# Kernel optimization log

Measured on AMD Instinct MI355X. Metric: run time of the kernel, lower is better.

The kernel has to match this reference:

```python
import jax, jax.numpy as jnp
import numpy as np
from jax import lax

B, CIN, N = 4, 3, 2048
H, COUT, LEVELS = 128, 3, 3
HEADS = 8

# jnp.convolve(x, f, 'same') with len(f)=8 == correlation with f[::-1], x zero-padded (4,3).
# DWT then takes [::2], which is conv stride 2. IDWT zero-upsamples (lhs_dilation=2) then
# convolves 'same' with f[::-1], i.e. correlation with f, padding (4,4).

def _dwt(x, wlow, whigh):
    # x: (M, L) -> approx, detail each (M, L//2)
    rhs = jnp.stack([wlow[::-1], whigh[::-1]])[:, None, :]  # (2,1,8)
    out = lax.conv_general_dilated(x[:, None, :], rhs, window_strides=(2,),
                                   padding=[(4, 3)],
                                   dimension_numbers=('NCH', 'OIH', 'NCH'))
    return out[:, 0, :], out[:, 1, :]

def _idwt(a, d, wlow, whigh):
    # a, d: (M, L) -> (M, 2L); recon_low + recon_high fused as a 2-in-channel conv
    lhs = jnp.stack([a, d], axis=1)               # (M,2,L)
    rhs = jnp.stack([wlow, whigh])[None, :, :]    # (1,2,8)
    out = lax.conv_general_dilated(lhs, rhs, window_strides=(1,),
                                   padding=[(4, 4)], lhs_dilation=(2,),
                                   dimension_numbers=('NCH', 'OIH', 'NCH'))
    return out[:, 0, :]


def setup_inputs() -> dict:
    key = jax.random.key(0)
    ks = jax.random.split(key, 12)
    db4_low = jnp.array([0.23037781, 0.71484657, 0.63088076, -0.02798376,
                         -0.18703481, 0.03084138, 0.03288301, -0.0105974], jnp.float32)
    db4_high = jnp.array([-0.0105974, -0.03288301, 0.03084138, 0.18703481,
                          -0.02798376, -0.63088076, 0.71484657, -0.23037781], jnp.float32)
    def s(k, shape, fan_in):
        return jax.random.normal(k, shape, jnp.float32) * (1.0 / fan_in) ** 0.5
    return {
        'x': jax.random.normal(ks[0], (B, CIN, N), jnp.float32),
        'wlow': db4_low, 'whigh': db4_high,
        'Win': s(ks[1], (CIN, H), CIN), 'b_in': jnp.zeros((H,), jnp.float32),
        'W1': s(ks[2], (LEVELS, 2, 2 * H), 2), 'b1': jnp.zeros((LEVELS, 2 * H), jnp.float32),
        'W2': s(ks[3], (LEVELS, 2 * H, H), 2 * H), 'b2': jnp.zeros((LEVELS, H), jnp.float32),
        'Wq': s(ks[4], (H, H), H), 'bq': jnp.zeros((H,), jnp.float32),
        'Wk': s(ks[5], (H, H), H), 'bk': jnp.zeros((H,), jnp.float32),
        'Wv': s(ks[6], (H, H), H), 'bv': jnp.zeros((H,), jnp.float32),
        'Wo': s(ks[7], (H, H), H), 'bo': jnp.zeros((H,), jnp.float32),
        'Wout': s(ks[8], (H, COUT), H), 'bout': jnp.zeros((COUT,), jnp.float32),
    }


def reference(x, wlow, whigh, Win, b_in, W1, b1, W2, b2,
              Wq, bq, Wk, bk, Wv, bv, Wo, bo, Wout, bout):
    Bx = x.shape[0]
    # input projection: (B,CIN,N) -> (B,H,N)
    xp = jnp.einsum('bcn,ch->bhn', x, Win) + b_in[None, :, None]
    cur = xp.reshape(Bx * H, N)  # per-(batch,channel) 1D signals, fully batched
    proc = []  # processed coeffs per level; note approx == detail after the shared mean
    for lvl in range(LEVELS):
        a, d = _dwt(cur, wlow, whigh)                 # (M, L)
        c = jnp.stack([a, d], axis=-1)                # (M, L, 2)
        h = jax.nn.gelu(c @ W1[lvl] + b1[lvl])        # (M, L, 2H)
        p = (h @ W2[lvl] + b2[lvl]).mean(axis=-1)     # (M, L): mean over hidden dim
        proc.append(p)
        cur = a
    rec = proc[-1]  # start from deepest processed approx
    for lvl in range(LEVELS - 1, -1, -1):
        rec = _idwt(rec, proc[lvl], wlow, whigh)
    y = rec.reshape(Bx, H, N)
    # cross-level attention: standard MHA with embed_dim=H, 8 heads, no dropout
    seq = y.transpose(0, 2, 1)  # (B,N,H)
    dh = H // HEADS
    q = (seq @ Wq + bq).reshape(Bx, N, HEADS, dh)
    k = (seq @ Wk + bk).reshape(Bx, N, HEADS, dh)
    v = (seq @ Wv + bv).reshape(Bx, N, HEADS, dh)
    att = jnp.einsum('bqhd,bkhd->bhqk', q, k) * (dh ** -0.5)
    att = jax.nn.softmax(att, axis=-1)
    o = jnp.einsum('bhqk,bkhd->bqhd', att, v).reshape(Bx, N, H)
    o = o @ Wo + bo
    out = o @ Wout + bout  # (B,N,COUT)
    return out.transpose(0, 2, 1)  # (B,COUT,N)
```

## Files before the change

kernel.cpp:

```cpp
#include <hip/hip_runtime.h>

#define N_    2048
#define H_    128
#define B_    4
#define CIN_  3
#define COUT_ 3
#define LOG2E 1.44269504089f

__device__ __forceinline__ float gelu_tanh(float x) {
    float x2 = x * x;
    float e = __builtin_amdgcn_exp2f(x * fmaf(-0.10294340397f, x2, -2.30220899f));
    return x * __builtin_amdgcn_rcpf(1.0f + e);
}

__global__ void prep_kernel(const float* __restrict__ W1, const float* __restrict__ b1,
                            const float* __restrict__ W2, const float* __restrict__ b2,
                            const float* __restrict__ Wo, const float* __restrict__ bo,
                            const float* __restrict__ Wout, const float* __restrict__ bout,
                            float4* __restrict__ wpack, float* __restrict__ b2m,
                            float* __restrict__ wf, float* __restrict__ bf) {
    int gid = blockIdx.x * 256 + threadIdx.x;
    if (gid < 768) {
        const float* r = W2 + (size_t)gid * 128;
        float s = 0.f;
        for (int h = 0; h < 128; ++h) s += r[h];
        int lvl = gid >> 8, k = gid & 255;
        wpack[gid] = make_float4(W1[lvl * 512 + k], W1[lvl * 512 + 256 + k],
                                 b1[gid], s * (1.0f / 128.0f));
    } else if (gid < 771) {
        int lvl = gid - 768;
        const float* r = b2 + lvl * 128;
        float s = 0.f;
        for (int h = 0; h < 128; ++h) s += r[h];
        b2m[lvl] = s * (1.0f / 128.0f);
    } else if (gid >= 1024 && gid < 1408) {
        int e = gid - 1024;
        int h = e / 3, c = e - 3 * h;
        float s = 0.f;
        for (int j = 0; j < 128; ++j) s = fmaf(Wo[h * 128 + j], Wout[j * 3 + c], s);
        wf[e] = s;
    } else if (gid >= 1408 && gid < 1411) {
        int c = gid - 1408;
        float s = bout[c];
        for (int j = 0; j < 128; ++j) s = fmaf(bo[j], Wout[j * 3 + c], s);
        bf[c] = s;
    }
}

template<bool FUSEX>
__global__ __launch_bounds__(256) void dwt_mlp_kernel(
        const float* __restrict__ src, int loSh,
        const float* __restrict__ x, const float* __restrict__ Win,
        const float* __restrict__ b_in,
        const float* __restrict__ wlow, const float* __restrict__ whigh,
        const float4* __restrict__ wpack, const float* __restrict__ b2ml,
        float* __restrict__ a_out, float* __restrict__ p_out) {
    int tid = threadIdx.x;
    int gid = blockIdx.x * 256 + tid;
    int Lo  = 1 << loSh;
    int m   = gid >> loSh;
    int i   = gid & (Lo - 1);
    int L   = Lo << 1;
    int j0  = 2 * i - 4;
    float xw[8];
    if (FUSEX) {
        int b = m >> 7, h = m & 127;
        float w0 = Win[h], w1 = Win[128 + h], w2 = Win[256 + h];
        float bi = b_in[h];
        const float* xr = x + (size_t)b * (CIN_ * N_);
#pragma unroll
        for (int t = 0; t < 8; ++t) {
            int j = j0 + t;
            bool ok = (unsigned)j < (unsigned)L;
            int jc = ok ? j : 0;
            float v = bi;
            v = fmaf(xr[jc], w0, v);
            v = fmaf(xr[N_ + jc], w1, v);
            v = fmaf(xr[2 * N_ + jc], w2, v);
            xw[t] = ok ? v : 0.f;
        }
    } else {
        const float* row = src + (size_t)m * L;
#pragma unroll
        for (int t = 0; t < 8; ++t) {
            int j = j0 + t;
            xw[t] = ((unsigned)j < (unsigned)L) ? row[j] : 0.f;
        }
    }
    float a = 0.f, d = 0.f;
#pragma unroll
    for (int t = 0; t < 8; ++t) {
        a = fmaf(xw[t], wlow[7 - t], a);
        d = fmaf(xw[t], whigh[7 - t], d);
    }
    float acc = 0.f;
#pragma unroll 8
    for (int kk = 0; kk < 256; ++kk) {
        float4 w = wpack[kk];
        float t = fmaf(a, w.x, fmaf(d, w.y, w.z));
        acc = fmaf(gelu_tanh(t), w.w, acc);
    }
    a_out[gid] = a;
    p_out[gid] = acc + b2ml[0];
}

__global__ __launch_bounds__(256) void idwt_kernel(
        const float* __restrict__ aSrc, const float* __restrict__ dSrc,
        int loutSh, const float* __restrict__ wlow, const float* __restrict__ whigh,
        float* __restrict__ out) {
    int tid  = threadIdx.x;
    int gid  = blockIdx.x * 256 + tid;
    int Lout = 1 << loutSh;
    int L    = Lout >> 1;
    int m    = gid >> loutSh;
    int ii   = gid & (Lout - 1);
    const float* ar = aSrc + (size_t)m * L;
    const float* dr = dSrc + (size_t)m * L;
    int podd = ii & 1;
    int off0 = (ii >> 1) - 2 + podd;
    float wlp[4], whp[4];
#pragma unroll
    for (int s = 0; s < 4; ++s) {
        wlp[s] = podd ? wlow[2 * s + 1] : wlow[2 * s];
        whp[s] = podd ? whigh[2 * s + 1] : whigh[2 * s];
    }
    float r = 0.f;
#pragma unroll
    for (int s = 0; s < 4; ++s) {
        int idx = off0 + s;
        bool ok = (unsigned)idx < (unsigned)L;
        float av = ok ? ar[idx] : 0.f;
        float dv = ok ? dr[idx] : 0.f;
        r = fmaf(av, wlp[s], r);
        r = fmaf(dv, whp[s], r);
    }
    out[gid] = r;
}

__global__ __launch_bounds__(384) void qkv_kernel(
        const float* __restrict__ r0,
        const float* __restrict__ Wq, const float* __restrict__ bq,
        const float* __restrict__ Wk, const float* __restrict__ bk,
        const float* __restrict__ Wv, const float* __restrict__ bv,
        float* __restrict__ qB, float* __restrict__ kB, float* __restrict__ vB) {
    int tid = threadIdx.x;
    int rowbase = blockIdx.x * 16;
    int b  = rowbase >> 11;
    int n0 = rowbase & 2047;

    const float* W; const float* bias; float* dst; int jj;
    if (tid < 128)      { W = Wq; bias = bq; dst = qB; jj = tid; }
    else if (tid < 256) { W = Wk; bias = bk; dst = kB; jj = tid - 128; }
    else                { W = Wv; bias = bv; dst = vB; jj = tid - 256; }

    const float* abase = r0 + (size_t)b * (H_ * N_) + n0;
    float acc[16];
#pragma unroll
    for (int r = 0; r < 16; ++r) acc[r] = 0.f;
    for (int h = 0; h < 128; ++h) {
        float w = W[h * 128 + jj];
        const float* ar = abase + (size_t)h * N_;
#pragma unroll
        for (int r = 0; r < 16; ++r) acc[r] = fmaf(ar[r], w, acc[r]);
    }
    float bb = bias[jj];
    int head = jj >> 4, t = jj & 15;
    size_t obase = ((size_t)(b * 8 + head) * N_) * 16 + t;
#pragma unroll
    for (int r = 0; r < 16; ++r)
        dst[obase + (size_t)(n0 + r) * 16] = acc[r] + bb;
}

#define DOT4(acc, qq, aa) do { acc = fmaf(qq.x, aa.x, acc); acc = fmaf(qq.y, aa.y, acc); \
                               acc = fmaf(qq.z, aa.z, acc); acc = fmaf(qq.w, aa.w, acc); } while (0)
#define SCALE4(oo, c)     do { oo.x *= c; oo.y *= c; oo.z *= c; oo.w *= c; } while (0)
#define AXPY4(oo, p, aa)  do { oo.x = fmaf(p, aa.x, oo.x); oo.y = fmaf(p, aa.y, oo.y); \
                               oo.z = fmaf(p, aa.z, oo.z); oo.w = fmaf(p, aa.w, oo.w); } while (0)

template<int KS>
__global__ __launch_bounds__(128, 2) void attn_kernel(
        const float* __restrict__ qb, const float* __restrict__ kb,
        const float* __restrict__ vb,
        float* __restrict__ part_o, float* __restrict__ part_ml) {
    __shared__ float4 kt4[512];
    __shared__ float4 vt4[512];
    int tid   = threadIdx.x;
    int blk   = blockIdx.x;
    int split = blk % KS;
    int qblk  = (blk / KS) & 3;
    int bh    = blk / (4 * KS);

    const float4* ksrc = (const float4*)(kb + (size_t)bh * (N_ * 16));
    const float4* vsrc = (const float4*)(vb + (size_t)bh * (N_ * 16));
    const float sc = 0.25f * LOG2E;

    float4 q[4][4];
    float  m[4], l[4];
    float4 o[4][4];
#pragma unroll
    for (int qi = 0; qi < 4; ++qi) {
        const float4* qr = (const float4*)(qb + ((size_t)bh * N_ + qblk * 512 + qi * 128 + tid) * 16);
#pragma unroll
        for (int j = 0; j < 4; ++j) { q[qi][j] = qr[j]; SCALE4(q[qi][j], sc); }
        m[qi] = -3.0e38f; l[qi] = 0.f;
#pragma unroll
        for (int j = 0; j < 4; ++j) o[qi][j] = make_float4(0.f, 0.f, 0.f, 0.f);
    }

    int k0 = split * (N_ / KS);
    for (int t0 = k0; t0 < k0 + N_ / KS; t0 += 128) {
        __syncthreads();
        const float4* ks = ksrc + t0 * 4;
        const float4* vs = vsrc + t0 * 4;
#pragma unroll
        for (int u = 0; u < 4; ++u) {
            kt4[tid + u * 128] = ks[tid + u * 128];
            vt4[tid + u * 128] = vs[tid + u * 128];
        }
        __syncthreads();

        for (int c0 = 0; c0 < 128; c0 += 4) {
            float sv[4][4];
            float cm[4] = {-3.0e38f, -3.0e38f, -3.0e38f, -3.0e38f};
#pragma unroll
            for (int c = 0; c < 4; ++c) {
                int kr = (c0 + c) * 4;
                float4 k0v = kt4[kr], k1v = kt4[kr+1], k2v = kt4[kr+2], k3v = kt4[kr+3];
#pragma unroll
                for (int qi = 0; qi < 4; ++qi) {
                    float s0 = 0.f, s1 = 0.f;
                    DOT4(s0, q[qi][0], k0v); DOT4(s1, q[qi][1], k1v);
                    DOT4(s0, q[qi][2], k2v); DOT4(s1, q[qi][3], k3v);
                    sv[qi][c] = s0 + s1;
                    cm[qi] = fmaxf(cm[qi], sv[qi][c]);
                }
            }
            bool need = (cm[0] > m[0] + 8.f) || (cm[1] > m[1] + 8.f) ||
                        (cm[2] > m[2] + 8.f) || (cm[3] > m[3] + 8.f);
            if (__any(need)) {
#pragma unroll
                for (int qi = 0; qi < 4; ++qi) {
                    float mn = fmaxf(m[qi], cm[qi]);
                    float cr = __builtin_amdgcn_exp2f(m[qi] - mn);
                    l[qi] *= cr;
#pragma unroll
                    for (int j = 0; j < 4; ++j) SCALE4(o[qi][j], cr);
                    m[qi] = mn;
                }
            }
#pragma unroll
            for (int c = 0; c < 4; ++c) {
                int vr = (c0 + c) * 4;
                float4 v0 = vt4[vr], v1 = vt4[vr+1], v2 = vt4[vr+2], v3 = vt4[vr+3];
#pragma unroll
                for (int qi = 0; qi < 4; ++qi) {
                    float p = __builtin_amdgcn_exp2f(sv[qi][c] - m[qi]);
                    l[qi] += p;
                    AXPY4(o[qi][0], p, v0); AXPY4(o[qi][1], p, v1);
                    AXPY4(o[qi][2], p, v2); AXPY4(o[qi][3], p, v3);
                }
            }
        }
    }
#pragma unroll
    for (int qi = 0; qi < 4; ++qi) {
        int qg = bh * N_ + qblk * 512 + qi * 128 + tid;
        float4* po = (float4*)part_o + ((size_t)split * 65536 + qg) * 4;
        po[0] = o[qi][0]; po[1] = o[qi][1]; po[2] = o[qi][2]; po[3] = o[qi][3];
        ((float2*)part_ml)[(size_t)split * 65536 + qg] = make_float2(m[qi], l[qi]);
    }
}

template<int KS>
__global__ __launch_bounds__(512) void combine_final_kernel(
        const float* __restrict__ part_o, const float* __restrict__ part_ml,
        const float* __restrict__ wf, const float* __restrict__ bf,
        float* __restrict__ out) {
    __shared__ float ysh[64 * 129];
    int tid = threadIdx.x;
    int b = blockIdx.x >> 5, nb = blockIdx.x & 31;
    int head = tid >> 6, nl = tid & 63;
    int n = nb * 64 + nl;
    int qg = (b * 8 + head) * N_ + n;

    float m[KS], l[KS];
    float M = -3.0e38f;
#pragma unroll
    for (int s = 0; s < KS; ++s) {
        float2 ml = ((const float2*)part_ml)[(size_t)s * 65536 + qg];
        m[s] = ml.x; l[s] = ml.y;
        M = fmaxf(M, m[s]);
    }
    float w[KS], lt = 0.f;
#pragma unroll
    for (int s = 0; s < KS; ++s) {
        w[s] = __builtin_amdgcn_exp2f(m[s] - M);
        lt = fmaf(l[s], w[s], lt);
    }
    float inv = __builtin_amdgcn_rcpf(lt);
    float o[16];
#pragma unroll
    for (int j = 0; j < 16; ++j) o[j] = 0.f;
#pragma unroll
    for (int s = 0; s < KS; ++s) {
        const float4* po = (const float4*)part_o + ((size_t)s * 65536 + qg) * 4;
#pragma unroll
        for (int r = 0; r < 4; ++r) {
            float4 v = po[r];
            o[4*r+0] = fmaf(v.x, w[s], o[4*r+0]);
            o[4*r+1] = fmaf(v.y, w[s], o[4*r+1]);
            o[4*r+2] = fmaf(v.z, w[s], o[4*r+2]);
            o[4*r+3] = fmaf(v.w, w[s], o[4*r+3]);
        }
    }
    int col = head * 16;
#pragma unroll
    for (int j = 0; j < 16; ++j) ysh[nl * 129 + col + j] = o[j] * inv;
    __syncthreads();
    if (tid < 192) {
        int c = tid >> 6, nl2 = tid & 63;
        float acc = bf[c];
        const float* yr = ysh + nl2 * 129;
#pragma unroll 4
        for (int h = 0; h < 128; ++h) acc = fmaf(yr[h], wf[h * 3 + c], acc);
        out[((size_t)b * 3 + c) * N_ + nb * 64 + nl2] = acc;
    }
}

extern "C" void kernel_launch(void* const* d_in, const int* in_sizes, int n_in,
                              void* d_out, int out_size, void* d_ws, size_t ws_size,
                              hipStream_t stream) {
    const float* x    = (const float*)d_in[0];
    const float* wlow = (const float*)d_in[1];
    const float* whigh= (const float*)d_in[2];
    const float* Win  = (const float*)d_in[3];
    const float* b_in = (const float*)d_in[4];
    const float* W1   = (const float*)d_in[5];
    const float* b1   = (const float*)d_in[6];
    const float* W2   = (const float*)d_in[7];
    const float* b2   = (const float*)d_in[8];
    const float* Wq   = (const float*)d_in[9];
    const float* bq   = (const float*)d_in[10];
    const float* Wk   = (const float*)d_in[11];
    const float* bk   = (const float*)d_in[12];
    const float* Wv   = (const float*)d_in[13];
    const float* bv   = (const float*)d_in[14];
    const float* Wo   = (const float*)d_in[15];
    const float* bo   = (const float*)d_in[16];
    const float* Wout = (const float*)d_in[17];
    const float* bout = (const float*)d_in[18];
    float* out = (float*)d_out;
    (void)in_sizes; (void)n_in; (void)out_size;

    float* ws = (float*)d_ws;
    float* qBuf  = ws;
    float* kBuf  = ws + 1048576;
    float* vBuf  = ws + 2097152;
    float* base2 = ws + 3145728;
    float* a1 = base2;
    float* p0 = base2 + 524288;
    float* a2 = base2 + 1048576;
    float* p1 = base2 + 1310720;
    float* a3 = base2 + 1572864;
    float* p2 = base2 + 1703936;
    float* r2 = base2 + 1835008;
    float* r1 = base2 + 2097152;
    float* r0 = base2 + 2621440;

    const size_t need8 = (3145728ull + 8ull * 1048576 + 8ull * 131072 + 8192ull) * 4;
    int KS = (ws_size >= need8) ? 8 : 4;

    float* part_o  = base2;
    float* part_ml = base2 + (size_t)KS * 1048576;
    float* smalls  = part_ml + (size_t)KS * 131072;
    float4* wpack = (float4*)smalls;
    float* b2m = smalls + 3072;
    float* wf  = smalls + 3088;
    float* bf  = smalls + 3472;

    prep_kernel<<<8, 256, 0, stream>>>(W1, b1, W2, b2, Wo, bo, Wout, bout, wpack, b2m, wf, bf);

    dwt_mlp_kernel<true><<<2048, 256, 0, stream>>>(nullptr, 10, x, Win, b_in, wlow, whigh,
                                                   wpack + 0,   b2m + 0, a1, p0);
    dwt_mlp_kernel<false><<<1024, 256, 0, stream>>>(a1, 9, nullptr, nullptr, nullptr, wlow, whigh,
                                                    wpack + 256, b2m + 1, a2, p1);
    dwt_mlp_kernel<false><<<512, 256, 0, stream>>>(a2, 8, nullptr, nullptr, nullptr, wlow, whigh,
                                                   wpack + 512, b2m + 2, a3, p2);

    idwt_kernel<<<1024, 256, 0, stream>>>(p2, p2, 9,  wlow, whigh, r2);
    idwt_kernel<<<2048, 256, 0, stream>>>(r2, p1, 10, wlow, whigh, r1);
    idwt_kernel<<<4096, 256, 0, stream>>>(r1, p0, 11, wlow, whigh, r0);

    qkv_kernel<<<512, 384, 0, stream>>>(r0, Wq, bq, Wk, bk, Wv, bv, qBuf, kBuf, vBuf);

    if (KS == 8) {
        attn_kernel<8><<<32 * 4 * 8, 128, 0, stream>>>(qBuf, kBuf, vBuf, part_o, part_ml);
        combine_final_kernel<8><<<128, 512, 0, stream>>>(part_o, part_ml, wf, bf, out);
    } else {
        attn_kernel<4><<<32 * 4 * 4, 128, 0, stream>>>(qBuf, kBuf, vBuf, part_o, part_ml);
        combine_final_kernel<4><<<128, 512, 0, stream>>>(part_o, part_ml, wf, bf, out);
    }
}
```

Before: 358.4 us.

## Fuse wavelet DWT/MLP/IDWT levels into one kernel and restructure attention

Replaces the three DWT+MLP launches and three IDWT launches with a single kernel per (batch,channel) row that keeps all intermediate levels in shared memory and only writes the reconstructed row. Separately rewrites attention to use 64-thread blocks with two queries per thread, reading K/V rows directly from global memory instead of staging tiles in LDS. The fusion removes launch overhead and global round trips. The attention change trades LDS reuse and per-thread query reuse for more blocks and no barriers, which risks higher load traffic per key.

```diff
diff --git a/kernel.cpp b/kernel.cpp
--- a/kernel.cpp
+++ b/kernel.cpp
@@ -47,94 +47,175 @@
     }
 }
 
-template<bool FUSEX>
-__global__ __launch_bounds__(256) void dwt_mlp_kernel(
-        const float* __restrict__ src, int loSh,
+__global__ __launch_bounds__(256) void wavelet_fused_kernel(
         const float* __restrict__ x, const float* __restrict__ Win,
         const float* __restrict__ b_in,
         const float* __restrict__ wlow, const float* __restrict__ whigh,
-        const float4* __restrict__ wpack, const float* __restrict__ b2ml,
-        float* __restrict__ a_out, float* __restrict__ p_out) {
+        const float4* __restrict__ wpack, const float* __restrict__ b2m,
+        float* __restrict__ r0g) {
+    __shared__ float cur[2048];
+    __shared__ float aA[1024];
+    __shared__ float pp0[1024];
+    __shared__ float aB[512];
+    __shared__ float pp1[512];
+    __shared__ float pp2[256];
+    __shared__ float r2s[512];
+    __shared__ float r1s[1024];
     int tid = threadIdx.x;
-    int gid = blockIdx.x * 256 + tid;
-    int Lo  = 1 << loSh;
-    int m   = gid >> loSh;
-    int i   = gid & (Lo - 1);
-    int L   = Lo << 1;
-    int j0  = 2 * i - 4;
-    float xw[8];
-    if (FUSEX) {
-        int b = m >> 7, h = m & 127;
-        float w0 = Win[h], w1 = Win[128 + h], w2 = Win[256 + h];
-        float bi = b_in[h];
-        const float* xr = x + (size_t)b * (CIN_ * N_);
+    int m = blockIdx.x;
+    int b = m >> 7, h = m & 127;
+    float w0 = Win[h], w1 = Win[128 + h], w2 = Win[256 + h];
+    float bi = b_in[h];
+    float wl[8], wh[8];
+#pragma unroll
+    for (int t = 0; t < 8; ++t) { wl[t] = wlow[t]; wh[t] = whigh[t]; }
+
+    const float* xr = x + (size_t)b * (CIN_ * N_);
+    for (int idx = tid; idx < 2048; idx += 256) {
+        float v = bi;
+        v = fmaf(xr[idx], w0, v);
+        v = fmaf(xr[N_ + idx], w1, v);
+        v = fmaf(xr[2 * N_ + idx], w2, v);
+        cur[idx] = v;
+    }
+    __syncthreads();
+
+    {
+        float a4[4], d4[4], acc4[4];
+#pragma unroll
+        for (int u = 0; u < 4; ++u) {
+            int i = tid + u * 256;
+            int j0 = 2 * i - 4;
+            float a = 0.f, d = 0.f;
+#pragma unroll
+            for (int t = 0; t < 8; ++t) {
+                int j = j0 + t;
+                float xv = ((unsigned)j < 2048u) ? cur[j] : 0.f;
+                a = fmaf(xv, wl[7 - t], a);
+                d = fmaf(xv, wh[7 - t], d);
+            }
+            a4[u] = a; d4[u] = d; aA[i] = a; acc4[u] = 0.f;
+        }
+#pragma unroll 4
+        for (int kk = 0; kk < 256; ++kk) {
+            float4 w = wpack[kk];
+#pragma unroll
+            for (int u = 0; u < 4; ++u) {
+                float t = fmaf(a4[u], w.x, fmaf(d4[u], w.y, w.z));
+                acc4[u] = fmaf(gelu_tanh(t), w.w, acc4[u]);
+            }
+        }
+        float bb = b2m[0];
+#pragma unroll
+        for (int u = 0; u < 4; ++u) pp0[tid + u * 256] = acc4[u] + bb;
+    }
+    __syncthreads();
+
+    {
+        float a2v[2], d2v[2], acc2[2];
+#pragma unroll
+        for (int u = 0; u < 2; ++u) {
+            int i = tid + u * 256;
+            int j0 = 2 * i - 4;
+            float a = 0.f, d = 0.f;
+#pragma unroll
+            for (int t = 0; t < 8; ++t) {
+                int j = j0 + t;
+                float xv = ((unsigned)j < 1024u) ? aA[j] : 0.f;
+                a = fmaf(xv, wl[7 - t], a);
+                d = fmaf(xv, wh[7 - t], d);
+            }
+            a2v[u] = a; d2v[u] = d; aB[i] = a; acc2[u] = 0.f;
+        }
+#pragma unroll 4
+        for (int kk = 0; kk < 256; ++kk) {
+            float4 w = wpack[256 + kk];
+#pragma unroll
+            for (int u = 0; u < 2; ++u) {
+                float t = fmaf(a2v[u], w.x, fmaf(d2v[u], w.y, w.z));
+                acc2[u] = fmaf(gelu_tanh(t), w.w, acc2[u]);
+            }
+        }
+        float bb = b2m[1];
+#pragma unroll
+        for (int u = 0; u < 2; ++u) pp1[tid + u * 256] = acc2[u] + bb;
+    }
+    __syncthreads();
+
+    {
+        int j0 = 2 * tid - 4;
+        float a = 0.f, d = 0.f;
 #pragma unroll
         for (int t = 0; t < 8; ++t) {
             int j = j0 + t;
-            bool ok = (unsigned)j < (unsigned)L;
-            int jc = ok ? j : 0;
-            float v = bi;
-            v = fmaf(xr[jc], w0, v);
-            v = fmaf(xr[N_ + jc], w1, v);
-            v = fmaf(xr[2 * N_ + jc], w2, v);
-            xw[t] = ok ? v : 0.f;
-        }
-    } else {
-        const float* row = src + (size_t)m * L;
-#pragma unroll
-        for (int t = 0; t < 8; ++t) {
-            int j = j0 + t;
-            xw[t] = ((unsigned)j < (unsigned)L) ? row[j] : 0.f;
-        }
-    }
-    float a = 0.f, d = 0.f;
-#pragma unroll
-    for (int t = 0; t < 8; ++t) {
-        a = fmaf(xw[t], wlow[7 - t], a);
-        d = fmaf(xw[t], whigh[7 - t], d);
-    }
-    float acc = 0.f;
-#pragma unroll 8
-    for (int kk = 0; kk < 256; ++kk) {
-        float4 w = wpack[kk];
-        float t = fmaf(a, w.x, fmaf(d, w.y, w.z));
-        acc = fmaf(gelu_tanh(t), w.w, acc);
-    }
-    a_out[gid] = a;
-    p_out[gid] = acc + b2ml[0];
-}
-
-__global__ __launch_bounds__(256) void idwt_kernel(
-        const float* __restrict__ aSrc, const float* __restrict__ dSrc,
-        int loutSh, const float* __restrict__ wlow, const float* __restrict__ whigh,
-        float* __restrict__ out) {
-    int tid  = threadIdx.x;
-    int gid  = blockIdx.x * 256 + tid;
-    int Lout = 1 << loutSh;
-    int L    = Lout >> 1;
-    int m    = gid >> loutSh;
-    int ii   = gid & (Lout - 1);
-    const float* ar = aSrc + (size_t)m * L;
-    const float* dr = dSrc + (size_t)m * L;
-    int podd = ii & 1;
-    int off0 = (ii >> 1) - 2 + podd;
-    float wlp[4], whp[4];
-#pragma unroll
-    for (int s = 0; s < 4; ++s) {
-        wlp[s] = podd ? wlow[2 * s + 1] : wlow[2 * s];
-        whp[s] = podd ? whigh[2 * s + 1] : whigh[2 * s];
-    }
-    float r = 0.f;
-#pragma unroll
-    for (int s = 0; s < 4; ++s) {
-        int idx = off0 + s;
-        bool ok = (unsigned)idx < (unsigned)L;
-        float av = ok ? ar[idx] : 0.f;
-        float dv = ok ? dr[idx] : 0.f;
-        r = fmaf(av, wlp[s], r);
-        r = fmaf(dv, whp[s], r);
-    }
-    out[gid] = r;
+            float xv = ((unsigned)j < 512u) ? aB[j] : 0.f;
+            a = fmaf(xv, wl[7 - t], a);
+            d = fmaf(xv, wh[7 - t], d);
+        }
+        float acc = 0.f;
+#pragma unroll 4
+        for (int kk = 0; kk < 256; ++kk) {
+            float4 w = wpack[512 + kk];
+            float t = fmaf(a, w.x, fmaf(d, w.y, w.z));
+            acc = fmaf(gelu_tanh(t), w.w, acc);
+        }
+        pp2[tid] = acc + b2m[2];
+    }
+    __syncthreads();
+
+#pragma unroll
+    for (int u = 0; u < 2; ++u) {
+        int ii = tid + u * 256;
+        int podd = ii & 1;
+        int off0 = (ii >> 1) - 2 + podd;
+        float r = 0.f;
+#pragma unroll
+        for (int s = 0; s < 4; ++s) {
+            int idx = off0 + s;
+            float av = ((unsigned)idx < 256u) ? pp2[idx] : 0.f;
+            r = fmaf(av, wl[2 * s + podd] + wh[2 * s + podd], r);
+        }
+        r2s[ii] = r;
+    }
+    __syncthreads();
+
+#pragma unroll
+    for (int u = 0; u < 4; ++u) {
+        int ii = tid + u * 256;
+        int podd = ii & 1;
+        int off0 = (ii >> 1) - 2 + podd;
+        float r = 0.f;
+#pragma unroll
+        for (int s = 0; s < 4; ++s) {
+            int idx = off0 + s;
+            bool ok = (unsigned)idx < 512u;
+            float av = ok ? r2s[idx] : 0.f;
+            float dv = ok ? pp1[idx] : 0.f;
+            r = fmaf(av, wl[2 * s + podd], r);
+            r = fmaf(dv, wh[2 * s + podd], r);
+        }
+        r1s[ii] = r;
+    }
+    __syncthreads();
+
+    float* orow = r0g + (size_t)m * 2048;
+#pragma unroll
+    for (int u = 0; u < 8; ++u) {
+        int ii = tid + u * 256;
+        int podd = ii & 1;
+        int off0 = (ii >> 1) - 2 + podd;
+        float r = 0.f;
+#pragma unroll
+        for (int s = 0; s < 4; ++s) {
+            int idx = off0 + s;
+            bool ok = (unsigned)idx < 1024u;
+            float av = ok ? r1s[idx] : 0.f;
+            float dv = ok ? pp0[idx] : 0.f;
+            r = fmaf(av, wl[2 * s + podd], r);
+            r = fmaf(dv, wh[2 * s + podd], r);
+        }
+        orow[ii] = r;
+    }
 }
 
 __global__ __launch_bounds__(384) void qkv_kernel(
@@ -178,97 +259,66 @@
                                oo.z = fmaf(p, aa.z, oo.z); oo.w = fmaf(p, aa.w, oo.w); } while (0)
 
 template<int KS>
-__global__ __launch_bounds__(128, 2) void attn_kernel(
+__global__ __launch_bounds__(64, 3) void attn_kernel(
         const float* __restrict__ qb, const float* __restrict__ kb,
         const float* __restrict__ vb,
         float* __restrict__ part_o, float* __restrict__ part_ml) {
-    __shared__ float4 kt4[512];
-    __shared__ float4 vt4[512];
-    int tid   = threadIdx.x;
+    int lane  = threadIdx.x;
     int blk   = blockIdx.x;
     int split = blk % KS;
-    int qblk  = (blk / KS) & 3;
-    int bh    = blk / (4 * KS);
-
-    const float4* ksrc = (const float4*)(kb + (size_t)bh * (N_ * 16));
-    const float4* vsrc = (const float4*)(vb + (size_t)bh * (N_ * 16));
+    int qblk  = (blk / KS) & 15;
+    int bh    = blk / (16 * KS);
+    int nA    = qblk * 128 + lane;
+    int nB    = nA + 64;
+
     const float sc = 0.25f * LOG2E;
-
-    float4 q[4][4];
-    float  m[4], l[4];
-    float4 o[4][4];
-#pragma unroll
-    for (int qi = 0; qi < 4; ++qi) {
-        const float4* qr = (const float4*)(qb + ((size_t)bh * N_ + qblk * 512 + qi * 128 + tid) * 16);
-#pragma unroll
-        for (int j = 0; j < 4; ++j) { q[qi][j] = qr[j]; SCALE4(q[qi][j], sc); }
-        m[qi] = -3.0e38f; l[qi] = 0.f;
-#pragma unroll
-        for (int j = 0; j < 4; ++j) o[qi][j] = make_float4(0.f, 0.f, 0.f, 0.f);
-    }
-
+    const float4* qra = (const float4*)(qb + ((size_t)bh * N_ + nA) * 16);
+    const float4* qrb = (const float4*)(qb + ((size_t)bh * N_ + nB) * 16);
+    float4 qa0 = qra[0], qa1 = qra[1], qa2 = qra[2], qa3 = qra[3];
+    float4 qb0 = qrb[0], qb1 = qrb[1], qb2 = qrb[2], qb3 = qrb[3];
+    SCALE4(qa0, sc); SCALE4(qa1, sc); SCALE4(qa2, sc); SCALE4(qa3, sc);
+    SCALE4(qb0, sc); SCALE4(qb1, sc); SCALE4(qb2, sc); SCALE4(qb3, sc);
+
+    float mA = -3.0e38f, lA = 0.f, mB = -3.0e38f, lB = 0.f;
+    float4 oA0 = {0,0,0,0}, oA1 = oA0, oA2 = oA0, oA3 = oA0;
+    float4 oB0 = oA0, oB1 = oA0, oB2 = oA0, oB3 = oA0;
+
+    const float* kbase = kb + (size_t)bh * (N_ * 16);
+    const float* vbase = vb + (size_t)bh * (N_ * 16);
     int k0 = split * (N_ / KS);
-    for (int t0 = k0; t0 < k0 + N_ / KS; t0 += 128) {
-        __syncthreads();
-        const float4* ks = ksrc + t0 * 4;
-        const float4* vs = vsrc + t0 * 4;
-#pragma unroll
-        for (int u = 0; u < 4; ++u) {
-            kt4[tid + u * 128] = ks[tid + u * 128];
-            vt4[tid + u * 128] = vs[tid + u * 128];
-        }
-        __syncthreads();
-
-        for (int c0 = 0; c0 < 128; c0 += 4) {
-            float sv[4][4];
-            float cm[4] = {-3.0e38f, -3.0e38f, -3.0e38f, -3.0e38f};
-#pragma unroll
-            for (int c = 0; c < 4; ++c) {
-                int kr = (c0 + c) * 4;
-                float4 k0v = kt4[kr], k1v = kt4[kr+1], k2v = kt4[kr+2], k3v = kt4[kr+3];
-#pragma unroll
-                for (int qi = 0; qi < 4; ++qi) {
-                    float s0 = 0.f, s1 = 0.f;
-                    DOT4(s0, q[qi][0], k0v); DOT4(s1, q[qi][1], k1v);
-                    DOT4(s0, q[qi][2], k2v); DOT4(s1, q[qi][3], k3v);
-                    sv[qi][c] = s0 + s1;
-                    cm[qi] = fmaxf(cm[qi], sv[qi][c]);
-                }
-            }
-            bool need = (cm[0] > m[0] + 8.f) || (cm[1] > m[1] + 8.f) ||
-                        (cm[2] > m[2] + 8.f) || (cm[3] > m[3] + 8.f);
-            if (__any(need)) {
-#pragma unroll
-                for (int qi = 0; qi < 4; ++qi) {
-                    float mn = fmaxf(m[qi], cm[qi]);
-                    float cr = __builtin_amdgcn_exp2f(m[qi] - mn);
-                    l[qi] *= cr;
-#pragma unroll
-                    for (int j = 0; j < 4; ++j) SCALE4(o[qi][j], cr);
-                    m[qi] = mn;
-                }
-            }
-#pragma unroll
-            for (int c = 0; c < 4; ++c) {
-                int vr = (c0 + c) * 4;
-                float4 v0 = vt4[vr], v1 = vt4[vr+1], v2 = vt4[vr+2], v3 = vt4[vr+3];
-#pragma unroll
-                for (int qi = 0; qi < 4; ++qi) {
-                    float p = __builtin_amdgcn_exp2f(sv[qi][c] - m[qi]);
-                    l[qi] += p;
-                    AXPY4(o[qi][0], p, v0); AXPY4(o[qi][1], p, v1);
-                    AXPY4(o[qi][2], p, v2); AXPY4(o[qi][3], p, v3);
-                }
-            }
-        }
-    }
-#pragma unroll
-    for (int qi = 0; qi < 4; ++qi) {
-        int qg = bh * N_ + qblk * 512 + qi * 128 + tid;
-        float4* po = (float4*)part_o + ((size_t)split * 65536 + qg) * 4;
-        po[0] = o[qi][0]; po[1] = o[qi][1]; po[2] = o[qi][2]; po[3] = o[qi][3];
-        ((float2*)part_ml)[(size_t)split * 65536 + qg] = make_float2(m[qi], l[qi]);
-    }
+#pragma unroll 2
+    for (int t = k0; t < k0 + N_ / KS; ++t) {
+        const float4* kr = (const float4*)(kbase + (size_t)t * 16);
+        float4 k0v = kr[0], k1v = kr[1], k2v = kr[2], k3v = kr[3];
+        float sA0 = 0.f, sA1 = 0.f, sB0 = 0.f, sB1 = 0.f;
+        DOT4(sA0, qa0, k0v); DOT4(sA1, qa1, k1v); DOT4(sA0, qa2, k2v); DOT4(sA1, qa3, k3v);
+        DOT4(sB0, qb0, k0v); DOT4(sB1, qb1, k1v); DOT4(sB0, qb2, k2v); DOT4(sB1, qb3, k3v);
+        float sA = sA0 + sA1, sB = sB0 + sB1;
+        if (__any((sA > mA + 8.f) || (sB > mB + 8.f))) {
+            float mnA = fmaxf(mA, sA), mnB = fmaxf(mB, sB);
+            float cA = __builtin_amdgcn_exp2f(mA - mnA);
+            float cB = __builtin_amdgcn_exp2f(mB - mnB);
+            lA *= cA; lB *= cB;
+            SCALE4(oA0, cA); SCALE4(oA1, cA); SCALE4(oA2, cA); SCALE4(oA3, cA);
+            SCALE4(oB0, cB); SCALE4(oB1, cB); SCALE4(oB2, cB); SCALE4(oB3, cB);
+            mA = mnA; mB = mnB;
+        }
+        float pA = __builtin_amdgcn_exp2f(sA - mA);
+        float pB = __builtin_amdgcn_exp2f(sB - mB);
+        lA += pA; lB += pB;
+        const float4* vr = (const float4*)(vbase + (size_t)t * 16);
+        float4 v0 = vr[0], v1 = vr[1], v2 = vr[2], v3 = vr[3];
+        AXPY4(oA0, pA, v0); AXPY4(oA1, pA, v1); AXPY4(oA2, pA, v2); AXPY4(oA3, pA, v3);
+        AXPY4(oB0, pB, v0); AXPY4(oB1, pB, v1); AXPY4(oB2, pB, v2); AXPY4(oB3, pB, v3);
+    }
+
+    int qgA = bh * N_ + nA, qgB = bh * N_ + nB;
+    float4* poA = (float4*)part_o + ((size_t)split * 65536 + qgA) * 4;
+    poA[0] = oA0; poA[1] = oA1; poA[2] = oA2; poA[3] = oA3;
+    float4* poB = (float4*)part_o + ((size_t)split * 65536 + qgB) * 4;
+    poB[0] = oB0; poB[1] = oB1; poB[2] = oB2; poB[3] = oB3;
+    ((float2*)part_ml)[(size_t)split * 65536 + qgA] = make_float2(mA, lA);
+    ((float2*)part_ml)[(size_t)split * 65536 + qgB] = make_float2(mB, lB);
 }
 
 template<int KS>
@@ -357,17 +407,9 @@
     float* kBuf  = ws + 1048576;
     float* vBuf  = ws + 2097152;
     float* base2 = ws + 3145728;
-    float* a1 = base2;
-    float* p0 = base2 + 524288;
-    float* a2 = base2 + 1048576;
-    float* p1 = base2 + 1310720;
-    float* a3 = base2 + 1572864;
-    float* p2 = base2 + 1703936;
-    float* r2 = base2 + 1835008;
-    float* r1 = base2 + 2097152;
-    float* r0 = base2 + 2621440;
-
-    const size_t need8 = (3145728ull + 8ull * 1048576 + 8ull * 131072 + 8192ull) * 4;
+    float* r0    = base2;
+
+    const size_t need8 = (3145728ull + 8ull * 1048576 + 8ull * 131072 + 4096ull) * 4;
     int KS = (ws_size >= need8) ? 8 : 4;
 
     float* part_o  = base2;
@@ -380,24 +422,16 @@
 
     prep_kernel<<<8, 256, 0, stream>>>(W1, b1, W2, b2, Wo, bo, Wout, bout, wpack, b2m, wf, bf);
 
-    dwt_mlp_kernel<true><<<2048, 256, 0, stream>>>(nullptr, 10, x, Win, b_in, wlow, whigh,
-                                                   wpack + 0,   b2m + 0, a1, p0);
-    dwt_mlp_kernel<false><<<1024, 256, 0, stream>>>(a1, 9, nullptr, nullptr, nullptr, wlow, whigh,
-                                                    wpack + 256, b2m + 1, a2, p1);
-    dwt_mlp_kernel<false><<<512, 256, 0, stream>>>(a2, 8, nullptr, nullptr, nullptr, wlow, whigh,
-                                                   wpack + 512, b2m + 2, a3, p2);
-
-    idwt_kernel<<<1024, 256, 0, stream>>>(p2, p2, 9,  wlow, whigh, r2);
-    idwt_kernel<<<2048, 256, 0, stream>>>(r2, p1, 10, wlow, whigh, r1);
-    idwt_kernel<<<4096, 256, 0, stream>>>(r1, p0, 11, wlow, whigh, r0);
+    wavelet_fused_kernel<<<512, 256, 0, stream>>>(x, Win, b_in, wlow, whigh,
+                                                  wpack, b2m, r0);
 
     qkv_kernel<<<512, 384, 0, stream>>>(r0, Wq, bq, Wk, bk, Wv, bv, qBuf, kBuf, vBuf);
 
     if (KS == 8) {
-        attn_kernel<8><<<32 * 4 * 8, 128, 0, stream>>>(qBuf, kBuf, vBuf, part_o, part_ml);
+        attn_kernel<8><<<32 * 16 * 8, 64, 0, stream>>>(qBuf, kBuf, vBuf, part_o, part_ml);
         combine_final_kernel<8><<<128, 512, 0, stream>>>(part_o, part_ml, wf, bf, out);
     } else {
-        attn_kernel<4><<<32 * 4 * 4, 128, 0, stream>>>(qBuf, kBuf, vBuf, part_o, part_ml);
+        attn_kernel<4><<<32 * 16 * 4, 64, 0, stream>>>(qBuf, kBuf, vBuf, part_o, part_ml);
         combine_final_kernel<4><<<128, 512, 0, stream>>>(part_o, part_ml, wf, bf, out);
     }
 }
```

Measured after the change: 395.6 us. +10.4%, slower.
